# Optimization experiments

Measured on AMD Instinct MI355X. Metric: run time of the kernel, lower is better.

## Reference

```python
import jax, jax.numpy as jnp
import numpy as np

B, L, H, F, K, NBINS, T = 32, 512, 512, 512, 3, 256, 4096
EPS = 1e-8  # RMSNorm epsilon
PAD = (K - 1) // 2  # =1, matches both conv paddings in the torch module


def _conv1d(x, w, b):
    # x: [B, L, Cin], w: [K, Cin, Cout]
    return jax.lax.conv_general_dilated(
        x, w, window_strides=(1,), padding=[(PAD, PAD)],
        dimension_numbers=('NLC', 'LIO', 'NLC')) + b


def _rms(x, g):
    return g * x / (jnp.sqrt(jnp.mean(x * x, axis=-1, keepdims=True)) + EPS)


def _vpred(x, mask, w1, b1, g1, w2, b2, g2, wl, bl):
    h = _rms(jax.nn.relu(_conv1d(x, w1, b1)), g1)
    h = _rms(jax.nn.relu(_conv1d(h, w2, b2)), g2)
    out = (h @ wl + bl)[..., 0]  # [B, L]
    return jnp.where(mask, 0.0, out)


def _proj(x, w1, b1, w2, b2):
    return jax.nn.relu(jax.nn.relu(x @ w1 + b1) @ w2 + b2)


def _length_regulate(x, dur, max_len):
    # Vectorized equivalent of LengthRegulator: repeat phoneme i dur[b,i] times, pad to max_len.
    cum = jnp.cumsum(dur, axis=1)               # [B, L]
    mel_len = cum[:, -1]                        # [B]
    t = jnp.arange(max_len)                     # [T]
    idx = jax.vmap(lambda c: jnp.searchsorted(c, t, side='right'))(cum)  # [B, T]
    idx = jnp.minimum(idx, x.shape[1] - 1)
    out = jnp.take_along_axis(x, idx[:, :, None], axis=1)  # [B, T, H]
    valid = (t[None, :] < mel_len[:, None])
    return out * valid[:, :, None].astype(x.dtype), mel_len


def setup_inputs() -> dict:
    key = jax.random.key(0)
    ks = iter(jax.random.split(key, 64))
    n = lambda *s: jax.random.normal(next(ks), s, jnp.float32) * 0.05
    inp = {}
    inp['x'] = jax.random.normal(next(ks), (B, L, H), jnp.float32)
    inp['embedding'] = jax.random.normal(next(ks), (B, L, H), jnp.float32)
    inp['src_mask'] = jnp.zeros((B, L), bool)
    inp['duration_target'] = jax.random.randint(next(ks), (B, L), 0, 9, jnp.int32)
    inp['pitch_target'] = jax.random.normal(next(ks), (B, L), jnp.float32)
    inp['energy_target'] = jax.random.normal(next(ks), (B, L), jnp.float32)
    inp['max_len'] = T
    for p in ['dur', 'pit', 'eng']:
        inp[p + '_w1'] = n(K, H, F); inp[p + '_b1'] = jnp.zeros(F, jnp.float32)
        inp[p + '_g1'] = jnp.ones(F, jnp.float32)
        inp[p + '_w2'] = n(K, F, F); inp[p + '_b2'] = jnp.zeros(F, jnp.float32)
        inp[p + '_g2'] = jnp.ones(F, jnp.float32)
        inp[p + '_wl'] = n(F, 1); inp[p + '_bl'] = jnp.zeros(1, jnp.float32)
    for p in ['pp', 'ep', 'sp']:
        inp[p + '_w1'] = n(H, H); inp[p + '_b1'] = jnp.zeros(H, jnp.float32)
        inp[p + '_w2'] = n(H, H); inp[p + '_b2'] = jnp.zeros(H, jnp.float32)
    inp['pitch_bins'] = jnp.linspace(-3.0, 3.0, NBINS - 1)
    inp['energy_bins'] = jnp.linspace(-3.0, 3.0, NBINS - 1)
    inp['pitch_emb'] = n(NBINS, H)
    inp['energy_emb'] = n(NBINS, H)
    return inp


def reference(x, embedding, src_mask, duration_target, pitch_target, energy_target, max_len,
              dur_w1, dur_b1, dur_g1, dur_w2, dur_b2, dur_g2, dur_wl, dur_bl,
              pit_w1, pit_b1, pit_g1, pit_w2, pit_b2, pit_g2, pit_wl, pit_bl,
              eng_w1, eng_b1, eng_g1, eng_w2, eng_b2, eng_g2, eng_wl, eng_bl,
              pp_w1, pp_b1, pp_w2, pp_b2,
              ep_w1, ep_b1, ep_w2, ep_b2,
              sp_w1, sp_b1, sp_w2, sp_b2,
              pitch_bins, energy_bins, pitch_emb, energy_emb):
    log_dur = _vpred(x, src_mask, dur_w1, dur_b1, dur_g1, dur_w2, dur_b2, dur_g2, dur_wl, dur_bl)
    pit_pred = _vpred(x + _proj(embedding, pp_w1, pp_b1, pp_w2, pp_b2), src_mask,
                      pit_w1, pit_b1, pit_g1, pit_w2, pit_b2, pit_g2, pit_wl, pit_bl)
    pitch_embedding = pitch_emb[jnp.searchsorted(pitch_bins, pitch_target)]  # torch.bucketize right=False == side='left'
    eng_pred = _vpred(x + _proj(embedding, ep_w1, ep_b1, ep_w2, ep_b2), src_mask,
                      eng_w1, eng_b1, eng_g1, eng_w2, eng_b2, eng_g2, eng_wl, eng_bl)
    energy_embedding = energy_emb[jnp.searchsorted(energy_bins, energy_target)]
    xo = x + energy_embedding + pitch_embedding + _proj(embedding, sp_w1, sp_b1, sp_w2, sp_b2)
    out, mel_len = _length_regulate(xo, duration_target, max_len)
    return (out, pit_pred, eng_pred, log_dur, mel_len)
```

## Files before the change

kernel.cpp:

```cpp
#include <hip/hip_runtime.h>

#define Bv    32
#define Lv    512
#define Hv    512
#define Fv    512
#define Tv    4096
#define Mv    (Bv*Lv)
#define NBINSv 256

#define OUT_OFF 0
#define PIT_OFF (Bv*(size_t)Tv*Hv)
#define ENG_OFF (PIT_OFF + Mv)
#define DUR_OFF (ENG_OFF + Mv)
#define MEL_OFF (DUR_OFF + Mv)

typedef unsigned short ushort;
typedef __attribute__((ext_vector_type(8))) short   bf16x8;
typedef __attribute__((ext_vector_type(4))) float   f32x4;
typedef __attribute__((ext_vector_type(8))) unsigned short u16x8;

__device__ __forceinline__ float b2f(ushort u) {
    union { float f; unsigned u; } x; x.u = ((unsigned)u) << 16; return x.f;
}
__device__ __forceinline__ ushort f2b(float f) {
    union { float f; unsigned u; } x; x.f = f;
    unsigned r = x.u + 0x7fffu + ((x.u >> 16) & 1u);
    return (ushort)(r >> 16);
}

#define GLL16(g, l) __builtin_amdgcn_global_load_lds( \
    (const __attribute__((address_space(1))) void*)(g), \
    (__attribute__((address_space(3))) void*)(l), 16, 0, 0)

template<int NZ> struct GArgs {
    const ushort* A[NZ];
    const ushort* W[NZ];
    const float*  bias[NZ];
    ushort*       C[NZ];
};
struct RmsArgs   { const ushort* h[3]; const float* g[3]; ushort* o[3]; };
struct RlArgs    { const ushort* h[3]; const float* g[3]; const float* wl[3]; const float* bl[3]; };
struct TransArgs { const float* src[6]; ushort* dst[6]; };
struct ConvArgs  { const float* src[2]; ushort* dst[2]; };

template<int NTAPS, int EPI, int NZ>
__global__ __launch_bounds__(256) void gemm_bf16_kernel(
    GArgs<NZ> ga, const float* __restrict__ res, const float* __restrict__ pe,
    const float* __restrict__ ee, const int* __restrict__ idxp,
    const int* __restrict__ idxe, const ushort* __restrict__ zp)
{
    constexpr int KTOT = NTAPS * 512;
    const int z = (NZ > 1) ? blockIdx.z : 0;
    const ushort* __restrict__ A    = ga.A[z];
    const ushort* __restrict__ Bt   = ga.W[z];
    const float*  __restrict__ bias = ga.bias[z];
    ushort*       __restrict__ C    = ga.C[z];

    __shared__ ushort As[128 * 32];
    __shared__ ushort Bs[128 * 32];

    const int tid = threadIdx.x;
    const int n0 = blockIdx.x * 128;
    const int m0 = blockIdx.y * 128;

    const int sar = tid >> 2;
    const int sl  = tid & 3;

    const int lane = tid & 63;
    const int w    = tid >> 6;
    const int wm   = (w & 1) * 64;
    const int wn   = (w >> 1) * 64;
    const int lr   = lane & 15;
    const int q    = lane >> 4;

    f32x4 acc[4][4];
    #pragma unroll
    for (int i = 0; i < 4; ++i)
        #pragma unroll
        for (int j = 0; j < 4; ++j) {
            f32x4 zz = {0.f, 0.f, 0.f, 0.f};
            acc[i][j] = zz;
        }

    for (int kt = 0; kt < NTAPS * 16; ++kt) {
        const int tap = (NTAPS == 3) ? (kt >> 4) : 0;
        const int kin = (NTAPS == 3) ? ((kt & 15) << 5) : (kt << 5);

        #pragma unroll
        for (int r = 0; r < 2; ++r) {
            const int row = sar + r * 64;
            const int m   = m0 + row;
            const int qg  = (sl - (row >> 1)) & 3;
            const ushort* asrc;
            if (NTAPS == 3) {
                const int l  = m & (Lv - 1);
                const int ls = l + tap - 1;
                asrc = ((unsigned)ls < (unsigned)Lv)
                     ? A + (size_t)(m + tap - 1) * 512 + kin + qg * 8
                     : zp;
            } else {
                asrc = A + (size_t)m * 512 + kin + qg * 8;
            }
            GLL16(asrc, &As[row * 32 + sl * 8]);
            const ushort* bsrc = Bt + (size_t)(n0 + row) * KTOT + tap * 512 + kin + qg * 8;
            GLL16(bsrc, &Bs[row * 32 + sl * 8]);
        }
        __syncthreads();

        bf16x8 af[4], bfr[4];
        #pragma unroll
        for (int i = 0; i < 4; ++i) {
            const int rm = wm + i * 16 + lr;
            af[i]  = *(const bf16x8*)&As[rm * 32 + (((q + (rm >> 1)) & 3) << 3)];
            const int rn = wn + i * 16 + lr;
            bfr[i] = *(const bf16x8*)&Bs[rn * 32 + (((q + (rn >> 1)) & 3) << 3)];
        }
        #pragma unroll
        for (int i = 0; i < 4; ++i)
            #pragma unroll
            for (int j = 0; j < 4; ++j)
                acc[i][j] = __builtin_amdgcn_mfma_f32_16x16x32_bf16(
                                af[i], bfr[j], acc[i][j], 0, 0, 0);
        __syncthreads();
    }

    #pragma unroll
    for (int i = 0; i < 4; ++i) {
        #pragma unroll
        for (int r = 0; r < 4; ++r) {
            const int m = m0 + wm + i * 16 + q * 4 + r;
            const size_t ro = (size_t)m * 512;
            int ip = 0, ie = 0;
            if (EPI == 2) { ip = idxp[m]; ie = idxe[m]; }
            #pragma unroll
            for (int j = 0; j < 4; ++j) {
                const int n = n0 + wn + j * 16 + lr;
                float v = acc[i][j][r] + bias[n];
                v = fmaxf(v, 0.f);
                if (EPI >= 1) v += res[ro + n];
                if (EPI == 2) v += pe[(size_t)ip * 512 + n] + ee[(size_t)ie * 512 + n];
                C[ro + n] = f2b(v);
            }
        }
    }
}

__global__ __launch_bounds__(256) void convert_kernel(ConvArgs ca)
{
    const float* __restrict__ X  = ca.src[blockIdx.y];
    ushort*      __restrict__ Xb = ca.dst[blockIdx.y];
    const size_t i = (size_t)blockIdx.x * 256 + threadIdx.x;
    const float4 a = ((const float4*)X)[2 * i];
    const float4 b = ((const float4*)X)[2 * i + 1];
    u16x8 o;
    o[0] = f2b(a.x); o[1] = f2b(a.y); o[2] = f2b(a.z); o[3] = f2b(a.w);
    o[4] = f2b(b.x); o[5] = f2b(b.y); o[6] = f2b(b.z); o[7] = f2b(b.w);
    *(u16x8*)(Xb + i * 8) = o;
}

__global__ __launch_bounds__(256) void transpose_kernel(TransArgs ta, int Ktot)
{
    const float* __restrict__ W  = ta.src[blockIdx.z];
    ushort*      __restrict__ Wt = ta.dst[blockIdx.z];
    __shared__ float t[32][33];
    const int k0 = blockIdx.x * 32, n0 = blockIdx.y * 32;
    const int r = threadIdx.x >> 5, c = threadIdx.x & 31;
    #pragma unroll
    for (int rr = 0; rr < 4; ++rr)
        t[r + rr * 8][c] = W[(size_t)(k0 + r + rr * 8) * 512 + n0 + c];
    __syncthreads();
    #pragma unroll
    for (int rr = 0; rr < 4; ++rr)
        Wt[(size_t)(n0 + r + rr * 8) * Ktot + k0 + c] = f2b(t[c][r + rr * 8]);
}

__global__ __launch_bounds__(128) void rms_kernel(RmsArgs ra)
{
    const int z = blockIdx.y;
    const int row = blockIdx.x;
    const int tid = threadIdx.x;
    const ushort* __restrict__ h = ra.h[z];
    const ushort4 hv = ((const ushort4*)(h + (size_t)row * 512))[tid];
    const float v0 = b2f(hv.x), v1 = b2f(hv.y), v2 = b2f(hv.z), v3 = b2f(hv.w);
    float ss = v0 * v0 + v1 * v1 + v2 * v2 + v3 * v3;
    #pragma unroll
    for (int off = 32; off; off >>= 1) ss += __shfl_down(ss, off, 64);
    __shared__ float p[2];
    if ((tid & 63) == 0) p[tid >> 6] = ss;
    __syncthreads();
    const float tot = p[0] + p[1];
    const float inv = 1.f / (sqrtf(tot * (1.f / 512.f)) + 1e-8f);
    const float4 gv = ((const float4*)ra.g[z])[tid];
    ushort4 ov;
    ov.x = f2b(gv.x * v0 * inv); ov.y = f2b(gv.y * v1 * inv);
    ov.z = f2b(gv.z * v2 * inv); ov.w = f2b(gv.w * v3 * inv);
    ((ushort4*)(ra.o[z] + (size_t)row * 512))[tid] = ov;
}

__global__ __launch_bounds__(256) void rmslin_kernel(
    RlArgs ra, const unsigned char* __restrict__ mask, float* __restrict__ predbase)
{
    const int z = blockIdx.y;
    const int wave = threadIdx.x >> 6, lane = threadIdx.x & 63;
    const int row = blockIdx.x * 4 + wave;
    const ushort* __restrict__ h = ra.h[z];
    const bf16x8 hv = *(const bf16x8*)(h + (size_t)row * 512 + lane * 8);
    const float4 g0 = *(const float4*)(ra.g[z] + lane * 8);
    const float4 g1 = *(const float4*)(ra.g[z] + lane * 8 + 4);
    const float4 w0 = *(const float4*)(ra.wl[z] + lane * 8);
    const float4 w1 = *(const float4*)(ra.wl[z] + lane * 8 + 4);
    float hf[8];
    #pragma unroll
    for (int t = 0; t < 8; ++t) hf[t] = b2f((ushort)hv[t]);
    float ss = 0.f, sgw = 0.f;
    #pragma unroll
    for (int t = 0; t < 8; ++t) ss += hf[t] * hf[t];
    sgw += hf[0]*g0.x*w0.x + hf[1]*g0.y*w0.y + hf[2]*g0.z*w0.z + hf[3]*g0.w*w0.w;
    sgw += hf[4]*g1.x*w1.x + hf[5]*g1.y*w1.y + hf[6]*g1.z*w1.z + hf[7]*g1.w*w1.w;
    #pragma unroll
    for (int off = 32; off; off >>= 1) {
        ss  += __shfl_down(ss,  off, 64);
        sgw += __shfl_down(sgw, off, 64);
    }
    if (lane == 0) {
        const float inv = 1.f / (sqrtf(ss * (1.f / 512.f)) + 1e-8f);
        predbase[(size_t)z * Mv + row] = mask[row] ? 0.f : (sgw * inv + ra.bl[z][0]);
    }
}

__global__ __launch_bounds__(256) void idx_kernel(
    const float* __restrict__ pt, const float* __restrict__ et,
    const float* __restrict__ pbins, const float* __restrict__ ebins,
    int* __restrict__ idxp, int* __restrict__ idxe)
{
    __shared__ float pb[NBINSv - 1], ebn[NBINSv - 1];
    const int tid = threadIdx.x;
    if (tid < NBINSv - 1) { pb[tid] = pbins[tid]; ebn[tid] = ebins[tid]; }
    __syncthreads();
    const int m = blockIdx.x * 256 + tid;
    const float pv = pt[m], ev = et[m];
    int lo = 0, hi = NBINSv - 1;
    while (lo < hi) { int mid = (lo + hi) >> 1; if (pb[mid] < pv) lo = mid + 1; else hi = mid; }
    idxp[m] = lo;
    lo = 0; hi = NBINSv - 1;
    while (lo < hi) { int mid = (lo + hi) >> 1; if (ebn[mid] < ev) lo = mid + 1; else hi = mid; }
    idxe[m] = lo;
}

__global__ __launch_bounds__(512) void cumsum_kernel(
    const int* __restrict__ dur, int* __restrict__ cum,
    int* __restrict__ melint, float* __restrict__ melout)
{
    __shared__ int s[Lv];
    const int b = blockIdx.x, tid = threadIdx.x;
    s[tid] = dur[b * Lv + tid];
    __syncthreads();
    for (int off = 1; off < Lv; off <<= 1) {
        int t = (tid >= off) ? s[tid - off] : 0;
        __syncthreads();
        s[tid] += t;
        __syncthreads();
    }
    cum[b * Lv + tid] = s[tid];
    if (tid == Lv - 1) { melint[b] = s[tid]; melout[b] = (float)s[tid]; }
}

__global__ __launch_bounds__(256) void tmap_kernel(
    const int* __restrict__ cum, const int* __restrict__ melint,
    int* __restrict__ tmap)
{
    const int bt = blockIdx.x * 256 + threadIdx.x;
    const int b = bt >> 12;
    const int t = bt & (Tv - 1);
    const int* c = cum + b * Lv;
    int lo = 0, hi = Lv;
    while (lo < hi) { int mid = (lo + hi) >> 1; if (c[mid] <= t) lo = mid + 1; else hi = mid; }
    tmap[bt] = (t < melint[b]) ? (b * Lv + min(lo, Lv - 1)) : -1;
}

__global__ __launch_bounds__(128) void regulate_kernel(
    const ushort* __restrict__ xo, const int* __restrict__ tmap,
    float* __restrict__ out)
{
    const int bt = blockIdx.x;
    const int src = tmap[bt];
    float4 v = make_float4(0.f, 0.f, 0.f, 0.f);
    if (src >= 0) {
        const ushort4 u = ((const ushort4*)(xo + (size_t)src * 512))[threadIdx.x];
        v.x = b2f(u.x); v.y = b2f(u.y); v.z = b2f(u.z); v.w = b2f(u.w);
    }
    ((float4*)(out + (size_t)bt * 512))[threadIdx.x] = v;
}

extern "C" void kernel_launch(void* const* d_in, const int* in_sizes, int n_in,
                              void* d_out, int out_size, void* d_ws, size_t ws_size,
                              hipStream_t stream)
{
    const float* x    = (const float*)d_in[0];
    const float* emb  = (const float*)d_in[1];
    const unsigned char* mask = (const unsigned char*)d_in[2];
    const int*   durt = (const int*)d_in[3];
    const float* pt   = (const float*)d_in[4];
    const float* et   = (const float*)d_in[5];
    const float* dw1 = (const float*)d_in[7],  *db1 = (const float*)d_in[8],
               * dg1 = (const float*)d_in[9],  *dw2 = (const float*)d_in[10],
               * db2 = (const float*)d_in[11], *dg2 = (const float*)d_in[12],
               * dwl = (const float*)d_in[13], *dbl = (const float*)d_in[14];
    const float* pw1 = (const float*)d_in[15], *pb1 = (const float*)d_in[16],
               * pg1 = (const float*)d_in[17], *pw2 = (const float*)d_in[18],
               * pb2 = (const float*)d_in[19], *pg2 = (const float*)d_in[20],
               * pwl = (const float*)d_in[21], *pbl = (const float*)d_in[22];
    const float* ew1 = (const float*)d_in[23], *eb1 = (const float*)d_in[24],
               * eg1 = (const float*)d_in[25], *ew2 = (const float*)d_in[26],
               * eb2 = (const float*)d_in[27], *eg2 = (const float*)d_in[28],
               * ewl = (const float*)d_in[29], *ebl = (const float*)d_in[30];
    const float* ppw1 = (const float*)d_in[31], *ppb1 = (const float*)d_in[32],
               * ppw2 = (const float*)d_in[33], *ppb2 = (const float*)d_in[34];
    const float* epw1 = (const float*)d_in[35], *epb1 = (const float*)d_in[36],
               * epw2 = (const float*)d_in[37], *epb2 = (const float*)d_in[38];
    const float* spw1 = (const float*)d_in[39], *spb1 = (const float*)d_in[40],
               * spw2 = (const float*)d_in[41], *spb2 = (const float*)d_in[42];
    const float* pbins = (const float*)d_in[43];
    const float* ebins = (const float*)d_in[44];
    const float* pemb  = (const float*)d_in[45];
    const float* eemb  = (const float*)d_in[46];

    float* outf = (float*)d_out;

    int*    cum    = (int*)d_ws;
    int*    melint = cum + 16384;
    int*    idxp   = melint + 64;
    int*    idxe   = idxp + 16384;
    ushort* zp     = (ushort*)(idxe + 16384);
    int*    tmap   = idxe + 16448;
    ushort* xob    = (ushort*)((float*)d_ws + 262144);

    #define OBUF(i) ((ushort*)(outf + (size_t)(i) * 4194304))
    ushort* xb  = OBUF(0);   ushort* eb  = OBUF(1);
    ushort* pA0 = OBUF(2);   ushort* pA1 = OBUF(3);  ushort* pA2 = OBUF(4);
    ushort* xp  = OBUF(5);   ushort* xe  = OBUF(6);
    ushort* c0  = OBUF(7);   ushort* c1  = OBUF(8);  ushort* c2  = OBUF(9);
    ushort* r0  = OBUF(10);  ushort* r1  = OBUF(11); ushort* r2  = OBUF(12);
    ushort* wt[12];
    {
        size_t off = 13ull * 4194304;
        for (int i = 0; i < 6; ++i)  { wt[i] = (ushort*)(outf + off); off += 393216; }
        for (int i = 6; i < 12; ++i) { wt[i] = (ushort*)(outf + off); off += 131072; }
    }

    hipMemsetAsync(zp, 0, 64, stream);

    { ConvArgs ca = {{x, emb}, {xb, eb}};
      convert_kernel<<<dim3(4096, 2), 256, 0, stream>>>(ca); }
    { TransArgs ta = {{dw1, dw2, pw1, pw2, ew1, ew2}, {wt[0], wt[1], wt[2], wt[3], wt[4], wt[5]}};
      transpose_kernel<<<dim3(48, 16, 6), 256, 0, stream>>>(ta, 1536); }
    { TransArgs ta = {{ppw1, ppw2, epw1, epw2, spw1, spw2},
                      {wt[6], wt[7], wt[8], wt[9], wt[10], wt[11]}};
      transpose_kernel<<<dim3(16, 16, 6), 256, 0, stream>>>(ta, 512); }

    idx_kernel<<<Mv / 256, 256, 0, stream>>>(pt, et, pbins, ebins, idxp, idxe);
    cumsum_kernel<<<Bv, Lv, 0, stream>>>(durt, cum, melint, outf + MEL_OFF);
    tmap_kernel<<<Bv * Tv / 256, 256, 0, stream>>>(cum, melint, tmap);

    const dim3 g3(Fv / 128, Mv / 128, 3);
    const dim3 g2(Fv / 128, Mv / 128, 2);
    const dim3 g1(Fv / 128, Mv / 128, 1);

    { GArgs<3> a = {{eb, eb, eb}, {wt[6], wt[8], wt[10]}, {ppb1, epb1, spb1}, {pA0, pA1, pA2}};
      gemm_bf16_kernel<1, 0, 3><<<g3, 256, 0, stream>>>(a, nullptr, nullptr, nullptr,
                                                        nullptr, nullptr, zp); }
    { GArgs<2> a = {{pA0, pA1}, {wt[7], wt[9]}, {ppb2, epb2}, {xp, xe}};
      gemm_bf16_kernel<1, 1, 2><<<g2, 256, 0, stream>>>(a, x, nullptr, nullptr,
                                                        nullptr, nullptr, zp); }
    { GArgs<1> a = {{pA2}, {wt[11]}, {spb2}, {xob}};
      gemm_bf16_kernel<1, 2, 1><<<g1, 256, 0, stream>>>(a, x, pemb, eemb, idxp, idxe, zp); }

    { GArgs<3> a = {{xp, xe, xb}, {wt[2], wt[4], wt[0]}, {pb1, eb1, db1}, {c0, c1, c2}};
      gemm_bf16_kernel<3, 0, 3><<<g3, 256, 0, stream>>>(a, nullptr, nullptr, nullptr,
                                                        nullptr, nullptr, zp); }
    { RmsArgs ra = {{c0, c1, c2}, {pg1, eg1, dg1}, {r0, r1, r2}};
      rms_kernel<<<dim3(Mv, 3), 128, 0, stream>>>(ra); }
    { GArgs<3> a = {{r0, r1, r2}, {wt[3], wt[5], wt[1]}, {pb2, eb2, db2}, {c0, c1, c2}};
      gemm_bf16_kernel<3, 0, 3><<<g3, 256, 0, stream>>>(a, nullptr, nullptr, nullptr,
                                                        nullptr, nullptr, zp); }
    { RlArgs ra = {{c0, c1, c2}, {pg2, eg2, dg2}, {pwl, ewl, dwl}, {pbl, ebl, dbl}};
      rmslin_kernel<<<dim3(Mv / 4, 3), 256, 0, stream>>>(ra, mask, outf + PIT_OFF); }

    regulate_kernel<<<Bv * Tv, 128, 0, stream>>>(xob, tmap, outf + OUT_OFF);
}
```

Baseline: 844.9 us.

## Restructure GEMM loop by tap, transpose MFMA output for vector epilogue, fuse cumsum+tmap

Splits the GEMM K loop into an outer tap loop with hoisted row pointers, and drops the XOR swizzle on LDS reads and writes. MFMA operands are swapped so each lane holds four consecutive N columns, which lets the epilogue use float4 loads of bias, residual and embeddings and store ushort4. Cumsum and tmap computation are merged into one kernel that does the binary search over the shared-memory prefix sum, removing a launch and a global round trip. Removing the swizzle may bring back LDS bank conflicts on the fragment reads.

```diff
diff --git a/kernel.cpp b/kernel.cpp
--- a/kernel.cpp
+++ b/kernel.cpp
@@ -73,74 +73,90 @@
     const int lr   = lane & 15;
     const int q    = lane >> 4;
 
+    ushort* asd0 = &As[sar * 32 + sl * 8];
+    ushort* asd1 = &As[(sar + 64) * 32 + sl * 8];
+    ushort* bsd0 = &Bs[sar * 32 + sl * 8];
+    ushort* bsd1 = &Bs[(sar + 64) * 32 + sl * 8];
+
     f32x4 acc[4][4];
     #pragma unroll
-    for (int i = 0; i < 4; ++i)
+    for (int j = 0; j < 4; ++j)
         #pragma unroll
-        for (int j = 0; j < 4; ++j) {
+        for (int i = 0; i < 4; ++i) {
             f32x4 zz = {0.f, 0.f, 0.f, 0.f};
-            acc[i][j] = zz;
+            acc[j][i] = zz;
         }
 
-    for (int kt = 0; kt < NTAPS * 16; ++kt) {
-        const int tap = (NTAPS == 3) ? (kt >> 4) : 0;
-        const int kin = (NTAPS == 3) ? ((kt & 15) << 5) : (kt << 5);
-
+    for (int tap = 0; tap < NTAPS; ++tap) {
+        const ushort* ab[2];
         #pragma unroll
         for (int r = 0; r < 2; ++r) {
             const int row = sar + r * 64;
             const int m   = m0 + row;
-            const int qg  = (sl - (row >> 1)) & 3;
-            const ushort* asrc;
             if (NTAPS == 3) {
                 const int l  = m & (Lv - 1);
                 const int ls = l + tap - 1;
-                asrc = ((unsigned)ls < (unsigned)Lv)
-                     ? A + (size_t)(m + tap - 1) * 512 + kin + qg * 8
-                     : zp;
+                ab[r] = ((unsigned)ls < (unsigned)Lv)
+                      ? A + (size_t)(m + tap - 1) * 512 + sl * 8 : nullptr;
             } else {
-                asrc = A + (size_t)m * 512 + kin + qg * 8;
+                ab[r] = A + (size_t)m * 512 + sl * 8;
             }
-            GLL16(asrc, &As[row * 32 + sl * 8]);
-            const ushort* bsrc = Bt + (size_t)(n0 + row) * KTOT + tap * 512 + kin + qg * 8;
-            GLL16(bsrc, &Bs[row * 32 + sl * 8]);
         }
-        __syncthreads();
-
-        bf16x8 af[4], bfr[4];
-        #pragma unroll
-        for (int i = 0; i < 4; ++i) {
-            const int rm = wm + i * 16 + lr;
-            af[i]  = *(const bf16x8*)&As[rm * 32 + (((q + (rm >> 1)) & 3) << 3)];
-            const int rn = wn + i * 16 + lr;
-            bfr[i] = *(const bf16x8*)&Bs[rn * 32 + (((q + (rn >> 1)) & 3) << 3)];
-        }
-        #pragma unroll
-        for (int i = 0; i < 4; ++i)
+        const ushort* bb0 = Bt + (size_t)(n0 + sar) * KTOT + tap * 512 + sl * 8;
+        const ushort* bb1 = Bt + (size_t)(n0 + sar + 64) * KTOT + tap * 512 + sl * 8;
+
+        for (int kt = 0; kt < 16; ++kt) {
+            const int kin = kt << 5;
+            GLL16(ab[0] ? ab[0] + kin : zp, asd0);
+            GLL16(bb0 + kin, bsd0);
+            GLL16(ab[1] ? ab[1] + kin : zp, asd1);
+            GLL16(bb1 + kin, bsd1);
+            __syncthreads();
+
+            bf16x8 af[4], bfr[4];
+            #pragma unroll
+            for (int i = 0; i < 4; ++i) {
+                af[i]  = *(const bf16x8*)&As[(wm + i * 16 + lr) * 32 + q * 8];
+                bfr[i] = *(const bf16x8*)&Bs[(wn + i * 16 + lr) * 32 + q * 8];
+            }
             #pragma unroll
             for (int j = 0; j < 4; ++j)
-                acc[i][j] = __builtin_amdgcn_mfma_f32_16x16x32_bf16(
-                                af[i], bfr[j], acc[i][j], 0, 0, 0);
-        __syncthreads();
+                #pragma unroll
+                for (int i = 0; i < 4; ++i)
+                    acc[j][i] = __builtin_amdgcn_mfma_f32_16x16x32_bf16(
+                                    bfr[j], af[i], acc[j][i], 0, 0, 0);
+            __syncthreads();
+        }
     }
 
     #pragma unroll
     for (int i = 0; i < 4; ++i) {
+        const int m = m0 + wm + i * 16 + lr;
+        const size_t ro = (size_t)m * 512;
+        int ip = 0, ie = 0;
+        if (EPI == 2) { ip = idxp[m]; ie = idxe[m]; }
         #pragma unroll
-        for (int r = 0; r < 4; ++r) {
-            const int m = m0 + wm + i * 16 + q * 4 + r;
-            const size_t ro = (size_t)m * 512;
-            int ip = 0, ie = 0;
-            if (EPI == 2) { ip = idxp[m]; ie = idxe[m]; }
-            #pragma unroll
-            for (int j = 0; j < 4; ++j) {
-                const int n = n0 + wn + j * 16 + lr;
-                float v = acc[i][j][r] + bias[n];
-                v = fmaxf(v, 0.f);
-                if (EPI >= 1) v += res[ro + n];
-                if (EPI == 2) v += pe[(size_t)ip * 512 + n] + ee[(size_t)ie * 512 + n];
-                C[ro + n] = f2b(v);
+        for (int j = 0; j < 4; ++j) {
+            const int n = n0 + wn + j * 16 + q * 4;
+            const f32x4 a = acc[j][i];
+            const float4 bi = *(const float4*)(bias + n);
+            float v0 = fmaxf(a[0] + bi.x, 0.f);
+            float v1 = fmaxf(a[1] + bi.y, 0.f);
+            float v2 = fmaxf(a[2] + bi.z, 0.f);
+            float v3 = fmaxf(a[3] + bi.w, 0.f);
+            if (EPI >= 1) {
+                const float4 r4 = *(const float4*)(res + ro + n);
+                v0 += r4.x; v1 += r4.y; v2 += r4.z; v3 += r4.w;
             }
+            if (EPI == 2) {
+                const float4 p4 = *(const float4*)(pe + (size_t)ip * 512 + n);
+                const float4 e4 = *(const float4*)(ee + (size_t)ie * 512 + n);
+                v0 += p4.x + e4.x; v1 += p4.y + e4.y;
+                v2 += p4.z + e4.z; v3 += p4.w + e4.w;
+            }
+            ushort4 o4;
+            o4.x = f2b(v0); o4.y = f2b(v1); o4.z = f2b(v2); o4.w = f2b(v3);
+            *(ushort4*)(C + ro + n) = o4;
         }
     }
 }
@@ -247,9 +263,8 @@
     idxe[m] = lo;
 }
 
-__global__ __launch_bounds__(512) void cumsum_kernel(
-    const int* __restrict__ dur, int* __restrict__ cum,
-    int* __restrict__ melint, float* __restrict__ melout)
+__global__ __launch_bounds__(512) void cumtmap_kernel(
+    const int* __restrict__ dur, float* __restrict__ melout, int* __restrict__ tmap)
 {
     __shared__ int s[Lv];
     const int b = blockIdx.x, tid = threadIdx.x;
@@ -261,21 +276,15 @@
         s[tid] += t;
         __syncthreads();
     }
-    cum[b * Lv + tid] = s[tid];
-    if (tid == Lv - 1) { melint[b] = s[tid]; melout[b] = (float)s[tid]; }
-}
-
-__global__ __launch_bounds__(256) void tmap_kernel(
-    const int* __restrict__ cum, const int* __restrict__ melint,
-    int* __restrict__ tmap)
-{
-    const int bt = blockIdx.x * 256 + threadIdx.x;
-    const int b = bt >> 12;
-    const int t = bt & (Tv - 1);
-    const int* c = cum + b * Lv;
-    int lo = 0, hi = Lv;
-    while (lo < hi) { int mid = (lo + hi) >> 1; if (c[mid] <= t) lo = mid + 1; else hi = mid; }
-    tmap[bt] = (t < melint[b]) ? (b * Lv + min(lo, Lv - 1)) : -1;
+    const int mel = s[Lv - 1];
+    if (tid == 0) melout[b] = (float)mel;
+    #pragma unroll
+    for (int rr = 0; rr < Tv / 512; ++rr) {
+        const int t = tid + rr * 512;
+        int lo = 0, hi = Lv;
+        while (lo < hi) { int mid = (lo + hi) >> 1; if (s[mid] <= t) lo = mid + 1; else hi = mid; }
+        tmap[b * Tv + t] = (t < mel) ? (b * Lv + min(lo, Lv - 1)) : -1;
+    }
 }
 
 __global__ __launch_bounds__(128) void regulate_kernel(
@@ -327,9 +336,7 @@
 
     float* outf = (float*)d_out;
 
-    int*    cum    = (int*)d_ws;
-    int*    melint = cum + 16384;
-    int*    idxp   = melint + 64;
+    int*    idxp   = (int*)d_ws;
     int*    idxe   = idxp + 16384;
     ushort* zp     = (ushort*)(idxe + 16384);
     int*    tmap   = idxe + 16448;
@@ -359,8 +366,7 @@
       transpose_kernel<<<dim3(16, 16, 6), 256, 0, stream>>>(ta, 512); }
 
     idx_kernel<<<Mv / 256, 256, 0, stream>>>(pt, et, pbins, ebins, idxp, idxe);
-    cumsum_kernel<<<Bv, Lv, 0, stream>>>(durt, cum, melint, outf + MEL_OFF);
-    tmap_kernel<<<Bv * Tv / 256, 256, 0, stream>>>(cum, melint, tmap);
+    cumtmap_kernel<<<Bv, Lv, 0, stream>>>(durt, outf + MEL_OFF, tmap);
 
     const dim3 g3(Fv / 128, Mv / 128, 3);
     const dim3 g2(Fv / 128, Mv / 128, 2);
```

Result: slower. 880.7 us (+4.2%).
